# Kernel tuning notes

Measured on AMD Instinct MI355X. Metric: run time of the kernel, lower is better.

## Reference

```python
import jax, jax.numpy as jnp
import numpy as np

D_MODEL = 1024

def setup_inputs() -> dict:
    key = jax.random.key(0)
    ks = jax.random.split(key, 7)
    x = jax.random.normal(ks[0], (4, 2048, D_MODEL), dtype=jnp.float32)
    s = 1.0 / np.sqrt(D_MODEL)
    Wq = jax.random.uniform(ks[1], (D_MODEL, D_MODEL), jnp.float32, -s, s)
    bq = jax.random.uniform(ks[2], (D_MODEL,), jnp.float32, -s, s)
    Wk = jax.random.uniform(ks[3], (D_MODEL, D_MODEL), jnp.float32, -s, s)
    bk = jax.random.uniform(ks[4], (D_MODEL,), jnp.float32, -s, s)
    Wv = jax.random.uniform(ks[5], (D_MODEL, D_MODEL), jnp.float32, -s, s)
    bv = jax.random.uniform(ks[6], (D_MODEL,), jnp.float32, -s, s)
    return {"x": x, "Wq": Wq, "bq": bq, "Wk": Wk, "bk": bk, "Wv": Wv, "bv": bv}

def reference(x, Wq, bq, Wk, bk, Wv, bv):
    # single-head self-attention: q,k,v are [B, S, D]
    q = x @ Wq + bq
    k = x @ Wk + bk
    v = x @ Wv + bv
    scale = 1.0 / jnp.sqrt(jnp.asarray(D_MODEL, x.dtype))
    scores = jnp.einsum('bsd,btd->bst', q, k) * scale  # [B, S, S]
    attn = jax.nn.softmax(scores, axis=-1)
    return jnp.einsum('bst,btd->bsd', attn, v)
```

## Files before the change

### kernel.cpp

```cpp
#include <hip/hip_runtime.h>
#include <hip/hip_bf16.h>
#include <stdint.h>


typedef __attribute__((ext_vector_type(8))) short short8;
typedef __attribute__((ext_vector_type(4))) float f32x4;

__device__ __forceinline__ unsigned short f2bf(float f) {
  union { float f; uint32_t u; } c; c.f = f;
  uint32_t u = c.u;
  u += 0x7FFFu + ((u >> 16) & 1u);
  return (unsigned short)(u >> 16);
}

__device__ __forceinline__ void gl16(const void* g, void* l) {
  __builtin_amdgcn_global_load_lds(
      (const __attribute__((address_space(1))) unsigned int*)g,
      (__attribute__((address_space(3))) unsigned int*)l, 16, 0, 0);
}

__global__ __launch_bounds__(256) void k_qkv(
    const short* __restrict__ A, const short* __restrict__ B,
    short* __restrict__ Cb, short* __restrict__ vT,
    const float* __restrict__ b0, const float* __restrict__ b1,
    const float* __restrict__ b2)
{
  const int b = blockIdx.x;
  const int xcd = b & 7, r = b >> 3;
  const int z = r >> 6;
  const int mem = r & 63;
  const int tm = xcd * 8 + (mem >> 3);
  const int tn = mem & 7;

  __shared__ short lds[18432];

  const int tid  = threadIdx.x;
  const int lane = tid & 63;
  const int wid  = tid >> 6;
  const long tileM = (long)tm * 128;
  const long tileN = (long)tn * 128;
  const short* Az = A;
  const short* Bz = B + (long)z * 1048576L;

  const int c0 = tid, c1 = 256 + tid;
  const short* gA0 = Az + (tileM + (c0 >> 2)) * 1024 + (c0 & 3) * 8;
  const short* gA1 = Az + (tileM + (c1 >> 2)) * 1024 + (c1 & 3) * 8;
  const short* gB0 = Bz + (tileN + (c0 >> 2)) * 1024 + (c0 & 3) * 8;
  const short* gB1 = Bz + (tileN + (c1 >> 2)) * 1024 + (c1 & 3) * 8;

  const int fr = lane & 15, quad = lane >> 4;
  const int waveM = (wid >> 1) * 64, waveN = (wid & 1) * 64;

  f32x4 acc[4][4] = {};

  {
    short* base = lds;
    gl16(gA0, base + c0 * 8);
    gl16(gA1, base + c1 * 8);
    gl16(gB0, base + 4096 + c0 * 8);
    gl16(gB1, base + 4096 + c1 * 8);
  }

  for (int t = 0; t < 32; ++t) {
    __syncthreads();
    if (t + 1 < 32) {
      const int kt = (t + 1) << 5;
      short* base = lds + ((t + 1) & 1) * 8192;
      gl16(gA0 + kt, base + c0 * 8);
      gl16(gA1 + kt, base + c1 * 8);
      gl16(gB0 + kt, base + 4096 + c0 * 8);
      gl16(gB1 + kt, base + 4096 + c1 * 8);
    }
    const short* sA = lds + (t & 1) * 8192;
    const short* sB = sA + 4096;
    short8 af[4], bf[4];
#pragma unroll
    for (int i = 0; i < 4; ++i)
      af[i] = *(const short8*)&sA[(waveM + i * 16 + fr) * 32 + quad * 8];
#pragma unroll
    for (int j = 0; j < 4; ++j)
      bf[j] = *(const short8*)&sB[(waveN + j * 16 + fr) * 32 + quad * 8];
#pragma unroll
    for (int i = 0; i < 4; ++i)
#pragma unroll
      for (int j = 0; j < 4; ++j)
        acc[i][j] = __builtin_amdgcn_mfma_f32_16x16x32_bf16(af[i], bf[j],
                                                            acc[i][j], 0, 0, 0);
  }

  if (z == 2) {
    __syncthreads();
    short* scr = lds + wid * 4608;
#pragma unroll
    for (int j = 0; j < 4; ++j) {
      const float bv = b2[tileN + waveN + j * 16 + fr];
#pragma unroll
      for (int i = 0; i < 4; ++i)
#pragma unroll
        for (int r = 0; r < 4; ++r)
          scr[(j * 16 + fr) * 72 + i * 16 + quad * 4 + r] =
              (short)f2bf(acc[i][j][r] + bv);
    }
    const int gb = tm >> 4;
    const long t0 = (long)(tm & 15) * 128 + waveM;
#pragma unroll
    for (int c = 0; c < 8; ++c) {
      const int rr = c * 8 + (lane >> 3);
      const int cc = (lane & 7) * 8;
      short8 v = *(const short8*)&scr[rr * 72 + cc];
      const long gd = tileN + waveN + rr;
      *(short8*)(vT + ((long)gb << 21) + gd * 2048 + t0 + cc) = v;
    }
  } else {
    __syncthreads();
    short* scr = lds + wid * 4608;
    short* C = Cb + (long)z * 8388608L;
    const float* bias = (z == 0) ? b0 : b1;
#pragma unroll
    for (int j = 0; j < 4; ++j) {
      const float bv = bias[tileN + waveN + j * 16 + fr];
#pragma unroll
      for (int i = 0; i < 4; ++i)
#pragma unroll
        for (int r = 0; r < 4; ++r)
          scr[(i * 16 + quad * 4 + r) * 72 + j * 16 + fr] =
              (short)f2bf(acc[i][j][r] + bv);
    }
#pragma unroll
    for (int c = 0; c < 8; ++c) {
      const int row = c * 8 + (lane >> 3);
      const int col = (lane & 7) * 8;
      short8 v = *(const short8*)&scr[row * 72 + col];
      *(short8*)(C + (tileM + waveM + row) * 1024 + tileN + waveN + col) = v;
    }
  }
}

__global__ __launch_bounds__(1024) void k_score(
    const short* __restrict__ A, const short* __restrict__ B,
    short* __restrict__ Pp, float scale, float* __restrict__ rowsum)
{
  const int b = blockIdx.x;
  const int z = b >> 6;
  const int tm = (b & 63) >> 3, tn = b & 7;

  __shared__ short lds[32768];

  const int tid  = threadIdx.x;
  const int lane = tid & 63;
  const int wid  = tid >> 6;
  const long tileM = (long)tm * 256;
  const long tileN = (long)tn * 256;
  const short* Az = A + (long)z * 2097152L;
  const short* Bz = B + (long)z * 2097152L;

  const short* gA = Az + (tileM + (tid >> 2)) * 1024 + (tid & 3) * 8;
  const short* gB = Bz + (tileN + (tid >> 2)) * 1024 + (tid & 3) * 8;

  const int fr = lane & 15, quad = lane >> 4;
  const int waveM = (wid >> 2) * 64, waveN = (wid & 3) * 64;

  f32x4 acc[4][4] = {};

  {
    short* base = lds;
    gl16(gA, base + tid * 8);
    gl16(gB, base + 8192 + tid * 8);
  }

  for (int t = 0; t < 32; ++t) {
    __syncthreads();
    if (t + 1 < 32) {
      const int kt = (t + 1) << 5;
      short* base = lds + ((t + 1) & 1) * 16384;
      gl16(gA + kt, base + tid * 8);
      gl16(gB + kt, base + 8192 + tid * 8);
    }
    const short* sA = lds + (t & 1) * 16384;
    const short* sB = sA + 8192;
    short8 af[4], bf[4];
#pragma unroll
    for (int i = 0; i < 4; ++i)
      af[i] = *(const short8*)&sA[(waveM + i * 16 + fr) * 32 + quad * 8];
#pragma unroll
    for (int j = 0; j < 4; ++j)
      bf[j] = *(const short8*)&sB[(waveN + j * 16 + fr) * 32 + quad * 8];
#pragma unroll
    for (int i = 0; i < 4; ++i)
#pragma unroll
      for (int j = 0; j < 4; ++j)
        acc[i][j] = __builtin_amdgcn_mfma_f32_16x16x32_bf16(af[i], bf[j],
                                                            acc[i][j], 0, 0, 0);
  }

#pragma unroll
  for (int i = 0; i < 4; ++i)
#pragma unroll
    for (int j = 0; j < 4; ++j)
#pragma unroll
      for (int r = 0; r < 4; ++r)
        acc[i][j][r] = exp2f(acc[i][j][r] * scale);
#pragma unroll
  for (int i = 0; i < 4; ++i)
#pragma unroll
    for (int r = 0; r < 4; ++r) {
      float s = acc[i][0][r] + acc[i][1][r] + acc[i][2][r] + acc[i][3][r];
      s += __shfl_xor(s, 1);
      s += __shfl_xor(s, 2);
      s += __shfl_xor(s, 4);
      s += __shfl_xor(s, 8);
      if (fr == 0)
        atomicAdd(&rowsum[(long)z * 2048 + tileM + waveM + i * 16 + quad * 4 + r], s);
    }

  short* C = Pp + (long)z * 4194304L;
  const int wgrp = wid >> 2, wloc = wid & 3;
  for (int rnd = 0; rnd < 4; ++rnd) {
    __syncthreads();
    if (wgrp == rnd) {
      short* scr = lds + wloc * 4608;
#pragma unroll
      for (int j = 0; j < 4; ++j)
#pragma unroll
        for (int i = 0; i < 4; ++i)
#pragma unroll
          for (int r = 0; r < 4; ++r)
            scr[(i * 16 + quad * 4 + r) * 72 + j * 16 + fr] =
                (short)f2bf(acc[i][j][r]);
#pragma unroll
      for (int c = 0; c < 8; ++c) {
        const int row = c * 8 + (lane >> 3);
        const int col = (lane & 7) * 8;
        short8 v = *(const short8*)&scr[row * 72 + col];
        *(short8*)(C + (tileM + waveM + row) * 2048 + tileN + waveN + col) = v;
      }
    }
  }
}

__global__ __launch_bounds__(256) void k_pv(
    const short* __restrict__ A, const short* __restrict__ B,
    float* __restrict__ Cf, float* __restrict__ rowsum)
{
  const int b = blockIdx.x;
  const int s = b & 7, r0_ = b >> 3;
  const int z = r0_ >> 4;
  const int mem = r0_ & 15;
  const int tm = (s >> 1) * 4 + (mem >> 2);
  const int tn = (s & 1) * 4 + (mem & 3);

  __shared__ short lds[18432];

  const int tid  = threadIdx.x;
  const int lane = tid & 63;
  const int wid  = tid >> 6;
  const long tileM = (long)tm * 128;
  const long tileN = (long)tn * 128;
  const short* Az = A + (long)z * 4194304L;
  const short* Bz = B + (long)z * 2097152L;

  const int c0 = tid, c1 = 256 + tid;
  const short* gA0 = Az + (tileM + (c0 >> 2)) * 2048 + (c0 & 3) * 8;
  const short* gA1 = Az + (tileM + (c1 >> 2)) * 2048 + (c1 & 3) * 8;
  const short* gB0 = Bz + (tileN + (c0 >> 2)) * 2048 + (c0 & 3) * 8;
  const short* gB1 = Bz + (tileN + (c1 >> 2)) * 2048 + (c1 & 3) * 8;

  const int fr = lane & 15, quad = lane >> 4;
  const int waveM = (wid >> 1) * 64, waveN = (wid & 1) * 64;

  f32x4 acc[4][4] = {};

  {
    short* base = lds;
    gl16(gA0, base + c0 * 8);
    gl16(gA1, base + c1 * 8);
    gl16(gB0, base + 4096 + c0 * 8);
    gl16(gB1, base + 4096 + c1 * 8);
  }

  for (int t = 0; t < 64; ++t) {
    __syncthreads();
    if (t + 1 < 64) {
      const int kt = (t + 1) << 5;
      short* base = lds + ((t + 1) & 1) * 8192;
      gl16(gA0 + kt, base + c0 * 8);
      gl16(gA1 + kt, base + c1 * 8);
      gl16(gB0 + kt, base + 4096 + c0 * 8);
      gl16(gB1 + kt, base + 4096 + c1 * 8);
    }
    const short* sA = lds + (t & 1) * 8192;
    const short* sB = sA + 4096;
    short8 af[4], bf[4];
#pragma unroll
    for (int i = 0; i < 4; ++i)
      af[i] = *(const short8*)&sA[(waveM + i * 16 + fr) * 32 + quad * 8];
#pragma unroll
    for (int j = 0; j < 4; ++j)
      bf[j] = *(const short8*)&sB[(waveN + j * 16 + fr) * 32 + quad * 8];
#pragma unroll
    for (int i = 0; i < 4; ++i)
#pragma unroll
      for (int j = 0; j < 4; ++j)
        acc[i][j] = __builtin_amdgcn_mfma_f32_16x16x32_bf16(af[i], bf[j],
                                                            acc[i][j], 0, 0, 0);
  }

  float* C = Cf + (long)z * 2097152L;
#pragma unroll
  for (int i = 0; i < 4; ++i)
#pragma unroll
    for (int r = 0; r < 4; ++r) {
      const long gr = tileM + waveM + i * 16 + quad * 4 + r;
      const float rinv = 1.0f / rowsum[(long)z * 2048 + gr];
#pragma unroll
      for (int j = 0; j < 4; ++j)
        C[gr * 1024 + tileN + waveN + j * 16 + fr] = acc[i][j][r] * rinv;
    }
}

__global__ __launch_bounds__(256) void k_prep(
    const float4* __restrict__ x, ushort4* __restrict__ xb,
    const float* __restrict__ Wq, const float* __restrict__ Wk,
    const float* __restrict__ Wv, short* __restrict__ WT,
    float* __restrict__ rs)
{
  __shared__ short tile[32][33];
  const int b = blockIdx.x;
  if (b < 8192) {
    const long i = (long)b * 256 + threadIdx.x;
    float4 v = x[i];
    ushort4 o;
    o.x = f2bf(v.x); o.y = f2bf(v.y); o.z = f2bf(v.z); o.w = f2bf(v.w);
    xb[i] = o;
  } else if (b < 11264) {
    const int idx = b - 8192;
    const int z = idx >> 10, rem = idx & 1023;
    const float* W = (z == 0) ? Wq : ((z == 1) ? Wk : Wv);
    short* d = WT + (long)z * 1024 * 1024;
    const int n0 = (rem & 31) * 32, d0 = (rem >> 5) * 32;
    const int tx = threadIdx.x & 31, ty = threadIdx.x >> 5;
#pragma unroll
    for (int p = 0; p < 4; ++p)
      tile[ty + p * 8][tx] = (short)f2bf(W[(long)(d0 + ty + p * 8) * 1024 + n0 + tx]);
    __syncthreads();
#pragma unroll
    for (int p = 0; p < 4; ++p)
      d[(long)(n0 + ty + p * 8) * 1024 + d0 + tx] = tile[tx][ty + p * 8];
  } else {
#pragma unroll
    for (int p = 0; p < 32; ++p)
      rs[p * 256 + threadIdx.x] = 0.0f;
  }
}

extern "C" void kernel_launch(void* const* d_in, const int* in_sizes, int n_in,
                              void* d_out, int out_size, void* d_ws, size_t ws_size,
                              hipStream_t stream) {
  const float* x  = (const float*)d_in[0];
  const float* Wq = (const float*)d_in[1];
  const float* bq = (const float*)d_in[2];
  const float* Wk = (const float*)d_in[3];
  const float* bk = (const float*)d_in[4];
  const float* Wv = (const float*)d_in[5];
  const float* bv = (const float*)d_in[6];

  char* ws = (char*)d_ws;
  short* xb  = (short*)(ws);
  short* wt  = (short*)(ws + 16777216);
  short* qkv = (short*)(ws + 23068672);
  short* Pp  = (short*)(ws + 73400320);
  float* rs  = (float*)(ws + 106954752);
  short* vT  = qkv + 2L * 8388608;

  k_prep<<<11265, 256, 0, stream>>>((const float4*)x, (ushort4*)xb,
                                    Wq, Wk, Wv, wt, rs);
  k_qkv<<<1536, 256, 0, stream>>>(xb, wt, qkv, vT, bq, bk, bv);
  k_score<<<256, 1024, 0, stream>>>(qkv, qkv + 8388608, Pp,
                                    0.03125f * 1.44269504088896f, rs);
  k_pv<<<512, 256, 0, stream>>>(Pp, vT, (float*)d_out, rs);
}
```

Before: 250.2 us.

## Restructure score GEMM into 8-wave ping-pong pipeline with swizzled LDS and XCD mapping

The QK^T score kernel now runs 512 threads per block, and each wave computes a 128x64 tile instead of 64x64. The K step widens to 64 and the LDS double buffer uses an XOR swizzle against bank conflicts. The main loop is split into four MFMA phases interleaved with staged global-to-LDS loads, explicit vmcnt waits, raw barriers and s_setprio, so memory traffic overlaps compute. Blocks are remapped so each XCD handles contiguous row tiles for L2 reuse. The cost is a higher accumulator register count and more barriers, which could limit occupancy, and the hand-tuned waitcnt logic is fragile.

Measured after the change: 249.6 us. Within noise of the previous version (-0.2%).

```diff
diff --git a/kernel.cpp b/kernel.cpp
--- a/kernel.cpp
+++ b/kernel.cpp
@@ -18,6 +18,10 @@
       (const __attribute__((address_space(1))) unsigned int*)g,
       (__attribute__((address_space(3))) unsigned int*)l, 16, 0, 0);
 }
+
+#define FENCE() asm volatile("" ::: "memory")
+#define BARRIER() do { FENCE(); __builtin_amdgcn_s_barrier(); FENCE(); } while (0)
+#define VMWAIT(n) asm volatile("s_waitcnt vmcnt(" #n ")" ::: "memory")
 
 __global__ __launch_bounds__(256) void k_qkv(
     const short* __restrict__ A, const short* __restrict__ B,
@@ -136,72 +140,150 @@
   }
 }
 
-__global__ __launch_bounds__(1024) void k_score(
+__global__ __launch_bounds__(512, 2) void k_score(
     const short* __restrict__ A, const short* __restrict__ B,
     short* __restrict__ Pp, float scale, float* __restrict__ rowsum)
 {
+  __shared__ short lds[65536];
+
   const int b = blockIdx.x;
-  const int z = b >> 6;
-  const int tm = (b & 63) >> 3, tn = b & 7;
-
-  __shared__ short lds[32768];
-
-  const int tid  = threadIdx.x;
+  const int xcd = b & 7, jb = b >> 3;
+  const int p = xcd * 4 + (jb >> 3);
+  const int tn = jb & 7;
+  const int z = p >> 3, tm = p & 7;
+
+  const int tid = threadIdx.x;
   const int lane = tid & 63;
-  const int wid  = tid >> 6;
+  const int wid = tid >> 6;
+  const int fr = lane & 15, quad = lane >> 4;
+  const int wm = wid >> 2, wn = wid & 3;
+
   const long tileM = (long)tm * 256;
   const long tileN = (long)tn * 256;
   const short* Az = A + (long)z * 2097152L;
   const short* Bz = B + (long)z * 2097152L;
 
-  const short* gA = Az + (tileM + (tid >> 2)) * 1024 + (tid & 3) * 8;
-  const short* gB = Bz + (tileN + (tid >> 2)) * 1024 + (tid & 3) * 8;
-
-  const int fr = lane & 15, quad = lane >> 4;
-  const int waveM = (wid >> 2) * 64, waveN = (wid & 3) * 64;
-
-  f32x4 acc[4][4] = {};
-
-  {
-    short* base = lds;
-    gl16(gA, base + tid * 8);
-    gl16(gB, base + 8192 + tid * 8);
-  }
-
-  for (int t = 0; t < 32; ++t) {
-    __syncthreads();
-    if (t + 1 < 32) {
-      const int kt = (t + 1) << 5;
-      short* base = lds + ((t + 1) & 1) * 16384;
-      gl16(gA + kt, base + tid * 8);
-      gl16(gB + kt, base + 8192 + tid * 8);
-    }
-    const short* sA = lds + (t & 1) * 16384;
-    const short* sB = sA + 8192;
-    short8 af[4], bf[4];
-#pragma unroll
-    for (int i = 0; i < 4; ++i)
-      af[i] = *(const short8*)&sA[(waveM + i * 16 + fr) * 32 + quad * 8];
-#pragma unroll
-    for (int j = 0; j < 4; ++j)
-      bf[j] = *(const short8*)&sB[(waveN + j * 16 + fr) * 32 + quad * 8];
-#pragma unroll
-    for (int i = 0; i < 4; ++i)
-#pragma unroll
-      for (int j = 0; j < 4; ++j)
-        acc[i][j] = __builtin_amdgcn_mfma_f32_16x16x32_bf16(af[i], bf[j],
-                                                            acc[i][j], 0, 0, 0);
-  }
-
-#pragma unroll
-  for (int i = 0; i < 4; ++i)
+  const int srow = tid >> 3;
+  const int sslot = (tid & 7) ^ (srow & 7);
+  const short* gA = Az + (tileM + srow) * 1024 + sslot * 8;
+  const short* gB = Bz + (tileN + srow) * 1024 + sslot * 8;
+
+  const int frk = fr & 7;
+  const int aBase = wm << 13;
+  const int bRow  = 16384 + ((wn >> 1) << 13) + ((wn & 1) << 12);
+  const int o0 = ((quad ^ frk) << 3) + (fr << 6);
+  const int o1 = (((quad + 4) ^ frk) << 3) + (fr << 6);
+
+  f32x4 acc[8][4] = {};
+
+  auto stageA = [&](int tt) {
+    const short* s = gA + tt * 64;
+    short* d = &lds[(tt & 1) << 15];
+    gl16(s,          d + (tid << 3));
+    gl16(s + 65536,  d + 4096 + (tid << 3));
+    gl16(s + 131072, d + 8192 + (tid << 3));
+    gl16(s + 196608, d + 12288 + (tid << 3));
+  };
+  auto stageBh = [&](int tt, int h) {
+    const short* s = gB + tt * 64 + h * 131072;
+    short* d = &lds[((tt & 1) << 15) + 16384 + (h << 13)];
+    gl16(s,         d + (tid << 3));
+    gl16(s + 65536, d + 4096 + (tid << 3));
+  };
+
+  stageA(0); stageBh(0, 0); stageBh(0, 1); stageA(1);
+  VMWAIT(4);
+  BARRIER();
+
+#pragma unroll 1
+  for (int t = 0; t < 16; ++t) {
+    const int bb = (t & 1) << 15;
+    short8 af0[4][2], af1[4][2], bf0[2][2], bf1[2][2];
+
+#pragma unroll
+    for (int i = 0; i < 4; ++i) {
+      af0[i][0] = *(const short8*)&lds[bb + aBase + (i << 10) + o0];
+      af0[i][1] = *(const short8*)&lds[bb + aBase + (i << 10) + o1];
+    }
+#pragma unroll
+    for (int j = 0; j < 2; ++j) {
+      bf0[j][0] = *(const short8*)&lds[bb + bRow + (j << 10) + o0];
+      bf0[j][1] = *(const short8*)&lds[bb + bRow + (j << 10) + o1];
+    }
+    if (t + 1 < 16) stageBh(t + 1, 0);
+    BARRIER();
+    __builtin_amdgcn_s_setprio(1);
+#pragma unroll
+    for (int i = 0; i < 4; ++i)
+#pragma unroll
+      for (int j = 0; j < 2; ++j) {
+        acc[i][j] = __builtin_amdgcn_mfma_f32_16x16x32_bf16(af0[i][0], bf0[j][0], acc[i][j], 0, 0, 0);
+        acc[i][j] = __builtin_amdgcn_mfma_f32_16x16x32_bf16(af0[i][1], bf0[j][1], acc[i][j], 0, 0, 0);
+      }
+    __builtin_amdgcn_s_setprio(0);
+    BARRIER();
+
+#pragma unroll
+    for (int i = 0; i < 4; ++i) {
+      af1[i][0] = *(const short8*)&lds[bb + aBase + ((i + 4) << 10) + o0];
+      af1[i][1] = *(const short8*)&lds[bb + aBase + ((i + 4) << 10) + o1];
+    }
+    if (t + 1 < 16) stageBh(t + 1, 1);
+    BARRIER();
+    __builtin_amdgcn_s_setprio(1);
+#pragma unroll
+    for (int i = 0; i < 4; ++i)
+#pragma unroll
+      for (int j = 0; j < 2; ++j) {
+        acc[i + 4][j] = __builtin_amdgcn_mfma_f32_16x16x32_bf16(af1[i][0], bf0[j][0], acc[i + 4][j], 0, 0, 0);
+        acc[i + 4][j] = __builtin_amdgcn_mfma_f32_16x16x32_bf16(af1[i][1], bf0[j][1], acc[i + 4][j], 0, 0, 0);
+      }
+    __builtin_amdgcn_s_setprio(0);
+    BARRIER();
+
+#pragma unroll
+    for (int j = 0; j < 2; ++j) {
+      bf1[j][0] = *(const short8*)&lds[bb + bRow + ((j + 2) << 10) + o0];
+      bf1[j][1] = *(const short8*)&lds[bb + bRow + ((j + 2) << 10) + o1];
+    }
+    BARRIER();
+    __builtin_amdgcn_s_setprio(1);
+#pragma unroll
+    for (int i = 0; i < 4; ++i)
+#pragma unroll
+      for (int j = 0; j < 2; ++j) {
+        acc[i + 4][j + 2] = __builtin_amdgcn_mfma_f32_16x16x32_bf16(af1[i][0], bf1[j][0], acc[i + 4][j + 2], 0, 0, 0);
+        acc[i + 4][j + 2] = __builtin_amdgcn_mfma_f32_16x16x32_bf16(af1[i][1], bf1[j][1], acc[i + 4][j + 2], 0, 0, 0);
+      }
+    __builtin_amdgcn_s_setprio(0);
+    BARRIER();
+
+    if (t + 2 < 16) stageA(t + 2);
+    BARRIER();
+    __builtin_amdgcn_s_setprio(1);
+#pragma unroll
+    for (int i = 0; i < 4; ++i)
+#pragma unroll
+      for (int j = 0; j < 2; ++j) {
+        acc[i][j + 2] = __builtin_amdgcn_mfma_f32_16x16x32_bf16(af0[i][0], bf1[j][0], acc[i][j + 2], 0, 0, 0);
+        acc[i][j + 2] = __builtin_amdgcn_mfma_f32_16x16x32_bf16(af0[i][1], bf1[j][1], acc[i][j + 2], 0, 0, 0);
+      }
+    __builtin_amdgcn_s_setprio(0);
+    if (t < 14) { VMWAIT(4); } else { VMWAIT(0); }
+    BARRIER();
+  }
+
+#pragma unroll
+  for (int i = 0; i < 8; ++i)
 #pragma unroll
     for (int j = 0; j < 4; ++j)
 #pragma unroll
       for (int r = 0; r < 4; ++r)
         acc[i][j][r] = exp2f(acc[i][j][r] * scale);
-#pragma unroll
-  for (int i = 0; i < 4; ++i)
+
+  float* rsz = rowsum + (long)z * 2048 + tileM + wm * 128;
+#pragma unroll
+  for (int i = 0; i < 8; ++i)
 #pragma unroll
     for (int r = 0; r < 4; ++r) {
       float s = acc[i][0][r] + acc[i][1][r] + acc[i][2][r] + acc[i][3][r];
@@ -209,31 +291,29 @@
       s += __shfl_xor(s, 2);
       s += __shfl_xor(s, 4);
       s += __shfl_xor(s, 8);
-      if (fr == 0)
-        atomicAdd(&rowsum[(long)z * 2048 + tileM + waveM + i * 16 + quad * 4 + r], s);
-    }
-
+      if (fr == 0) atomicAdd(&rsz[i * 16 + quad * 4 + r], s);
+    }
+
+  __syncthreads();
   short* C = Pp + (long)z * 4194304L;
-  const int wgrp = wid >> 2, wloc = wid & 3;
-  for (int rnd = 0; rnd < 4; ++rnd) {
-    __syncthreads();
-    if (wgrp == rnd) {
-      short* scr = lds + wloc * 4608;
-#pragma unroll
-      for (int j = 0; j < 4; ++j)
-#pragma unroll
-        for (int i = 0; i < 4; ++i)
-#pragma unroll
-          for (int r = 0; r < 4; ++r)
-            scr[(i * 16 + quad * 4 + r) * 72 + j * 16 + fr] =
-                (short)f2bf(acc[i][j][r]);
-#pragma unroll
-      for (int c = 0; c < 8; ++c) {
-        const int row = c * 8 + (lane >> 3);
-        const int col = (lane & 7) * 8;
-        short8 v = *(const short8*)&scr[row * 72 + col];
-        *(short8*)(C + (tileM + waveM + row) * 2048 + tileN + waveN + col) = v;
-      }
+  short* scr = &lds[wid * 4608];
+#pragma unroll
+  for (int pass = 0; pass < 2; ++pass) {
+#pragma unroll
+    for (int j = 0; j < 4; ++j)
+#pragma unroll
+      for (int i = 0; i < 4; ++i)
+#pragma unroll
+        for (int r = 0; r < 4; ++r)
+          scr[(i * 16 + quad * 4 + r) * 72 + j * 16 + fr] =
+              (short)f2bf(acc[pass * 4 + i][j][r]);
+#pragma unroll
+    for (int c = 0; c < 8; ++c) {
+      const int row = c * 8 + (lane >> 3);
+      const int col = (lane & 7) * 8;
+      short8 v = *(const short8*)&scr[row * 72 + col];
+      *(short8*)(C + (tileM + wm * 128 + pass * 64 + row) * 2048 +
+                 tileN + wn * 64 + col) = v;
     }
   }
 }
@@ -375,7 +455,7 @@
   k_prep<<<11265, 256, 0, stream>>>((const float4*)x, (ushort4*)xb,
                                     Wq, Wk, Wv, wt, rs);
   k_qkv<<<1536, 256, 0, stream>>>(xb, wt, qkv, vT, bq, bk, bv);
-  k_score<<<256, 1024, 0, stream>>>(qkv, qkv + 8388608, Pp,
-                                    0.03125f * 1.44269504088896f, rs);
+  k_score<<<256, 512, 0, stream>>>(qkv, qkv + 8388608, Pp,
+                                   0.03125f * 1.44269504088896f, rs);
   k_pv<<<512, 256, 0, stream>>>(Pp, vT, (float*)d_out, rs);
 }
```
